# Performance work log

Measured on AMD Instinct MI355X. Metric: run time of the kernel, lower is better.

The kernel has to match this reference:

```python
import jax, jax.numpy as jnp
import numpy as np

B, S, D = 4, 4096, 64   # batch, seq_len, input_size
H, HD = 4, 16           # num_heads, head_dim


def setup_inputs() -> dict:
    key = jax.random.key(0)
    ks = jax.random.split(key, 9)
    sd = 1.0 / np.sqrt(D)          # torch Linear default uniform(-1/sqrt(fan_in), ...)
    so = 1.0 / np.sqrt(H * HD)
    u = lambda k, shape, s: jax.random.uniform(k, shape, jnp.float32, -s, s)
    return {
        "x": jax.random.normal(ks[0], (B, S, D), jnp.float32),
        "Wq": u(ks[1], (H, D, HD), sd), "bq": u(ks[2], (H, HD), sd),
        "Wk": u(ks[3], (H, D, HD), sd), "bk": u(ks[4], (H, HD), sd),
        "Wv": u(ks[5], (H, D, HD), sd), "bv": u(ks[6], (H, HD), sd),
        "Wo": u(ks[7], (H * HD, D), so), "bo": u(ks[8], (D,), so),
    }


def reference(x, Wq, bq, Wk, bk, Wv, bv, Wo, bo):
    # Batched per-head projections (fuses the original per-head Linear loop)
    q = jnp.einsum('bsd,hde->bhse', x, Wq) + bq[None, :, None, :]
    k = jnp.einsum('bsd,hde->bhse', x, Wk) + bk[None, :, None, :]
    v = jnp.einsum('bsd,hde->bhse', x, Wv) + bv[None, :, None, :]
    # scores: [B, H, S(query), S(key)]
    scores = jnp.einsum('bhse,bhte->bhst', q, k) / np.sqrt(HD).astype(np.float32)
    # FAITHFUL quirk: torch Softmax(dim=1) on [B,S,S] normalizes over the QUERY axis
    w = jax.nn.softmax(scores, axis=2)
    attended = jnp.einsum('bhst,bhte->bhse', w, v)          # [B,H,S,HD]
    concat = attended.transpose(0, 2, 1, 3).reshape(B, S, H * HD)
    out = concat @ Wo + bo                                   # [B,S,D]
    # FAITHFUL quirk: final softmax over the sequence axis (dim=1)
    return jax.nn.softmax(out, axis=1)
```

## Files before the change

### kernel.cpp

```cpp
#include <hip/hip_runtime.h>
#include <hip/hip_bf16.h>


#define BB 4
#define SS 4096
#define DD 64
#define HH 4
#define HDD 16

typedef unsigned int u32;
typedef unsigned short u16;
typedef __attribute__((ext_vector_type(8))) short bfrag;
typedef __attribute__((ext_vector_type(4))) float floatx4;
typedef __attribute__((ext_vector_type(16))) float floatx16;
typedef __attribute__((ext_vector_type(2))) u32 u32x2;
typedef __attribute__((ext_vector_type(4))) u32 u32x4;

#define LOG2E 1.4426950408889634074f
#define QSCALE (LOG2E * 0.25f)

__device__ __forceinline__ float fexp2(float x) {
#if __has_builtin(__builtin_amdgcn_exp2f)
  return __builtin_amdgcn_exp2f(x);
#else
  float r; asm("v_exp_f32 %0, %1" : "=v"(r) : "v"(x)); return r;
#endif
}
__device__ __forceinline__ float frcp(float x) {
#if __has_builtin(__builtin_amdgcn_rcpf)
  return __builtin_amdgcn_rcpf(x);
#else
  float r; asm("v_rcp_f32 %0, %1" : "=v"(r) : "v"(x)); return r;
#endif
}

__device__ __forceinline__ u16 f2bf(float f) {
  u32 u = __builtin_bit_cast(u32, f);
  return (u16)((u + 0x7FFFu + ((u >> 16) & 1u)) >> 16);
}
__device__ __forceinline__ u32 pack_bf(float lo, float hi) {
#if __has_builtin(__builtin_amdgcn_perm)
  return __builtin_amdgcn_perm(__builtin_bit_cast(u32, hi),
                               __builtin_bit_cast(u32, lo), 0x07060302u);
#else
  u32 a = __builtin_bit_cast(u32, lo);
  u32 b = __builtin_bit_cast(u32, hi);
  return (a >> 16) | (b & 0xFFFF0000u);
#endif
}

__global__ __launch_bounds__(256) void k_proj(
    const float* __restrict__ x,
    const float* __restrict__ Wq, const float* __restrict__ bq,
    const float* __restrict__ Wk, const float* __restrict__ bk,
    const float* __restrict__ Wv, const float* __restrict__ bv,
    u16* __restrict__ qb, u16* __restrict__ kb, float* __restrict__ vf)
{
  __shared__ float xs[16 * 64];
  const int tid = threadIdx.x;
  const int blk = blockIdx.x;
  const int b   = blk >> 8;
  const int s0  = (blk & 255) << 4;
  ((float4*)xs)[tid] = ((const float4*)(x + ((size_t)b * SS + s0) * DD))[tid];
  __syncthreads();

  const int col = tid & 63, h = col >> 4, e = col & 15;
  const int rg  = tid >> 6;
  float aq[4] = {0,0,0,0}, ak[4] = {0,0,0,0}, av[4] = {0,0,0,0};
  const int wofs = h * (DD * HDD) + e;
#pragma unroll 4
  for (int d = 0; d < DD; ++d) {
    float wq = Wq[wofs + d * HDD];
    float wk = Wk[wofs + d * HDD];
    float wv = Wv[wofs + d * HDD];
    const float* xr = xs + (rg * 4) * 64 + d;
#pragma unroll
    for (int r = 0; r < 4; ++r) {
      float xv = xr[r * 64];
      aq[r] += xv * wq; ak[r] += xv * wk; av[r] += xv * wv;
    }
  }
  const float bqv = bq[col], bkv = bk[col], bvv = bv[col];
  size_t base = ((size_t)(b * HH + h) * SS + (s0 + rg * 4)) * HDD + e;
#pragma unroll
  for (int r = 0; r < 4; ++r) {
    qb[base + r * HDD] = f2bf((aq[r] + bqv) * QSCALE);
    kb[base + r * HDD] = f2bf(ak[r] + bkv);
    vf[base + r * HDD] = av[r] + bvv;
  }
}

__global__ __launch_bounds__(256, 8) void k_colsum(
    const u16* __restrict__ qb, const u16* __restrict__ kb,
    float* __restrict__ csp)
{
  const int tid = threadIdx.x;
  const int lane = tid & 63, w = tid >> 6;
  const int l31 = lane & 31, hl = lane >> 5;
  const int bh = blockIdx.z, chunk = blockIdx.y;
  const int t0 = blockIdx.x * 128 + w * 32;
  const size_t base = (size_t)bh * (SS * HDD);

  const bfrag kf = *(const bfrag*)(kb + base + (size_t)(t0 + l31) * HDD + hl * 8);
  const u16* qp = qb + base + (size_t)l31 * HDD + hl * 8;
  const floatx16 z16 = {0.f};
  float c0 = 0.f, c1 = 0.f, c2 = 0.f, c3 = 0.f;
  const int s0 = chunk * 1024;
#pragma unroll 2
  for (int s = s0; s < s0 + 1024; s += 32) {
    bfrag qfr = *(const bfrag*)(qp + (size_t)s * HDD);
    floatx16 d = __builtin_amdgcn_mfma_f32_32x32x16_bf16(qfr, kf, z16, 0, 0, 0);
#pragma unroll
    for (int i = 0; i < 4; ++i) {
      c0 += fexp2(d[4 * i + 0]);
      c1 += fexp2(d[4 * i + 1]);
      c2 += fexp2(d[4 * i + 2]);
      c3 += fexp2(d[4 * i + 3]);
    }
  }
  float c = (c0 + c1) + (c2 + c3);
  c += __shfl_xor(c, 32, 64);
  if (hl == 0)
    csp[((size_t)bh * 4 + chunk) * SS + t0 + l31] = c;
}

__global__ __launch_bounds__(256, 4) void k_attn(
    const u16* __restrict__ qb, const u16* __restrict__ kb,
    const float* __restrict__ vf, const float* __restrict__ csp,
    float* __restrict__ attp)
{
  __shared__ __align__(16) u16 vls[2][16][264];
  __shared__ float rcs[2048];
  const int tid  = threadIdx.x;
  const int lane = tid & 63, w = tid >> 6;
  const int l31 = lane & 31, hl = lane >> 5;
  const int bh = blockIdx.z, b = bh >> 2, h = bh & 3;
  const int tph = blockIdx.y;
  const int s0 = blockIdx.x * 128 + w * 32;
  const size_t base = (size_t)bh * (SS * HDD);
  const int tbh = tph * 2048;

  {
    const float* cp0 = csp + (size_t)bh * 4 * SS + tbh;
#pragma unroll
    for (int i = 0; i < 8; ++i) {
      int j = i * 256 + tid;
      rcs[j] = frcp(cp0[j] + cp0[j + SS] + cp0[j + 2 * SS] + cp0[j + 3 * SS]);
    }
  }
  __syncthreads();

  const bfrag qf = *(const bfrag*)(qb + base + (size_t)(s0 + l31) * HDD + hl * 8);
  const u16* kp = kb + base + (size_t)l31 * HDD + hl * 8;
  const floatx16 z16 = {0.f};
  floatx16 acc = {0.f};

  const float4* vsrc = (const float4*)(vf + base + (size_t)tbh * HDD);

  {
#pragma unroll
    for (int kk = 0; kk < 4; ++kk) {
      int c = kk * 256 + tid;
      int tl = c >> 2, g = c & 3;
      float4 vv = vsrc[c];
      float rc = rcs[tl];
      int i5 = tl >> 5, t5 = tl & 31;
      int sub = ((t5 >> 2) & 1) * 16 + ((t5 >> 3) << 2) + (t5 & 3);
      u16* wp = &vls[0][0][0] + i5 * 32 + sub;
      wp[(4 * g + 0) * 264] = f2bf(vv.x * rc);
      wp[(4 * g + 1) * 264] = f2bf(vv.y * rc);
      wp[(4 * g + 2) * 264] = f2bf(vv.z * rc);
      wp[(4 * g + 3) * 264] = f2bf(vv.w * rc);
    }
  }
  __syncthreads();

#pragma unroll
  for (int ch = 0; ch < 8; ++ch) {
    float4 pv[4];
    if (ch < 7) {
#pragma unroll
      for (int kk = 0; kk < 4; ++kk)
        pv[kk] = vsrc[(ch + 1) * 1024 + kk * 256 + tid];
    }

    const u16* vrow = &vls[ch & 1][0][0] + (l31 & 15) * 264 + hl * 16;
    const int tb = tbh + ch * 256;
#pragma unroll 2
    for (int it = 0; it < 8; ++it) {
      bfrag kf = *(const bfrag*)(kp + (size_t)(tb + it * 32) * HDD);
      floatx16 d = __builtin_amdgcn_mfma_f32_32x32x16_bf16(kf, qf, z16, 0, 0, 0);
      u32 wr[8];
#pragma unroll
      for (int p = 0; p < 8; ++p)
        wr[p] = pack_bf(fexp2(d[2 * p]), fexp2(d[2 * p + 1]));
      const u16* va = vrow + it * 32;
      u32x4 af0 = *(const u32x4*)(va);
      u32x4 af1 = *(const u32x4*)(va + 8);
      u32x4 ef0 = {wr[0], wr[1], wr[2], wr[3]};
      u32x4 ef1 = {wr[4], wr[5], wr[6], wr[7]};
      acc = __builtin_amdgcn_mfma_f32_32x32x16_bf16(
          __builtin_bit_cast(bfrag, af0), __builtin_bit_cast(bfrag, ef0), acc, 0, 0, 0);
      acc = __builtin_amdgcn_mfma_f32_32x32x16_bf16(
          __builtin_bit_cast(bfrag, af1), __builtin_bit_cast(bfrag, ef1), acc, 0, 0, 0);
    }

    if (ch < 7) {
      u16* dstb = &vls[(ch + 1) & 1][0][0];
#pragma unroll
      for (int kk = 0; kk < 4; ++kk) {
        int c = kk * 256 + tid;
        int tl = c >> 2, g = c & 3;
        float rc = rcs[(ch + 1) * 256 + tl];
        int i5 = tl >> 5, t5 = tl & 31;
        int sub = ((t5 >> 2) & 1) * 16 + ((t5 >> 3) << 2) + (t5 & 3);
        u16* wp = dstb + i5 * 32 + sub;
        wp[(4 * g + 0) * 264] = f2bf(pv[kk].x * rc);
        wp[(4 * g + 1) * 264] = f2bf(pv[kk].y * rc);
        wp[(4 * g + 2) * 264] = f2bf(pv[kk].z * rc);
        wp[(4 * g + 3) * 264] = f2bf(pv[kk].w * rc);
      }
    }
    __syncthreads();
  }

  float* ao = attp + (((size_t)tph * BB + b) * SS + s0 + l31) * (HH * HDD)
            + h * HDD + 4 * hl;
  float4 lo4 = {acc[0], acc[1], acc[2], acc[3]};
  float4 hi4 = {acc[4], acc[5], acc[6], acc[7]};
  *(float4*)ao       = lo4;
  *(float4*)(ao + 8) = hi4;
}

__global__ __launch_bounds__(256) void k_oproj(
    const float* __restrict__ att, const float* __restrict__ Wo,
    const float* __restrict__ bo, float* __restrict__ outp,
    float* __restrict__ part)
{
  __shared__ float wols[64 * 64];
  __shared__ float red[4][64];
  const int tid = threadIdx.x;
  const int blk = blockIdx.x;
  const int b = blk >> 9, s0 = (blk & 511) << 3;
#pragma unroll
  for (int i = 0; i < 4; ++i)
    ((float4*)wols)[tid + 256 * i] = ((const float4*)Wo)[tid + 256 * i];
  __syncthreads();

  const int d = tid & 63, sg = tid >> 6;
  const float bov = bo[d];
  const size_t so = (size_t)BB * SS * 16;
  float es = 0.f;
#pragma unroll
  for (int r = 0; r < 2; ++r) {
    int s = s0 + sg * 2 + r;
    const floatx4* row = (const floatx4*)(att + ((size_t)b * SS + s) * 64);
    float acc = bov;
#pragma unroll
    for (int j = 0; j < 16; ++j) {
      floatx4 c = row[j] + row[j + so];
      acc += c[0] * wols[(4*j+0)*64 + d] + c[1] * wols[(4*j+1)*64 + d]
           + c[2] * wols[(4*j+2)*64 + d] + c[3] * wols[(4*j+3)*64 + d];
    }
    outp[((size_t)b * SS + s) * 64 + d] = acc;
    es += fexp2(acc * LOG2E);
  }
  red[sg][d] = es;
  __syncthreads();
  if (tid < 64)
    part[((size_t)b * 512 + (blk & 511)) * 64 + tid] =
        red[0][tid] + red[1][tid] + red[2][tid] + red[3][tid];
}

__global__ __launch_bounds__(256) void k_softmax(
    const float* __restrict__ outp, const float* __restrict__ part,
    float* __restrict__ out)
{
  __shared__ float red[4][64];
  __shared__ float rs[64];
  const int tid = threadIdx.x, d = tid & 63, sg = tid >> 6;
  const int st = blockIdx.x;
  const int b = blockIdx.y;
  {
    float e = 0.f;
    const float* pp = part + ((size_t)b * 512 + sg * 128) * 64 + d;
#pragma unroll 8
    for (int c = 0; c < 128; ++c) e += pp[c * 64];
    red[sg][d] = e;
  }
  __syncthreads();
  if (tid < 64)
    rs[tid] = frcp(red[0][tid] + red[1][tid] + red[2][tid] + red[3][tid]);
  __syncthreads();
  const float r = rs[d];
  const size_t rowbase = ((size_t)b * SS + st * 64 + sg * 16) * 64 + d;
#pragma unroll 4
  for (int i = 0; i < 16; ++i)
    out[rowbase + i * 64] = fexp2(outp[rowbase + i * 64] * LOG2E) * r;
}

extern "C" void kernel_launch(void* const* d_in, const int* in_sizes, int n_in,
                              void* d_out, int out_size, void* d_ws, size_t ws_size,
                              hipStream_t stream) {
  const float* x  = (const float*)d_in[0];
  const float* Wq = (const float*)d_in[1];
  const float* bq = (const float*)d_in[2];
  const float* Wk = (const float*)d_in[3];
  const float* bk = (const float*)d_in[4];
  const float* Wv = (const float*)d_in[5];
  const float* bv = (const float*)d_in[6];
  const float* Wo = (const float*)d_in[7];
  const float* bo = (const float*)d_in[8];

  char* ws = (char*)d_ws;
  constexpr size_t QB_OFF  = 0;
  constexpr size_t KB_OFF  = (size_t)2  << 20;
  constexpr size_t VF_OFF  = (size_t)4  << 20;
  constexpr size_t CSP_OFF = (size_t)10 << 20;
  constexpr size_t ATT_OFF = (size_t)11 << 20;
  constexpr size_t OUT_OFF = (size_t)27 << 20;
  constexpr size_t PT_OFF  = (size_t)31 << 20;

  u16*   qb   = (u16*)  (ws + QB_OFF);
  u16*   kb   = (u16*)  (ws + KB_OFF);
  float* vf   = (float*)(ws + VF_OFF);
  float* csp  = (float*)(ws + CSP_OFF);
  float* attp = (float*)(ws + ATT_OFF);
  float* outp = (float*)(ws + OUT_OFF);
  float* part = (float*)(ws + PT_OFF);
  float* out  = (float*)d_out;

  hipLaunchKernelGGL(k_proj,    dim3(1024),       dim3(256), 0, stream,
                     x, Wq, bq, Wk, bk, Wv, bv, qb, kb, vf);
  hipLaunchKernelGGL(k_colsum,  dim3(32, 4, 16),  dim3(256), 0, stream, qb, kb, csp);
  hipLaunchKernelGGL(k_attn,    dim3(32, 2, 16),  dim3(256), 0, stream,
                     qb, kb, vf, csp, attp);
  hipLaunchKernelGGL(k_oproj,   dim3(2048),       dim3(256), 0, stream,
                     attp, Wo, bo, outp, part);
  hipLaunchKernelGGL(k_softmax, dim3(64, 4),      dim3(256), 0, stream, outp, part, out);
}
```

Baseline: 184.2 us.

## Precompute scaled bf16 V tiles and stream them to LDS with direct loads

Adds a k_vprep kernel that scales V by the reciprocal column sums once, converts it to bf16 and writes it in a pre-swizzled tile layout. k_attn then copies those tiles straight into LDS with global_load_lds, which removes the per-block reciprocal computation and scattered scalar LDS stores. The key range is split into 4 parts instead of 2 to double the grid, and the launch bound is raised so more blocks fit per CU. The cost is an extra kernel launch, an extra pass over V in global memory, and four partial outputs that k_oproj must now sum.

```diff
diff --git a/kernel.cpp b/kernel.cpp
--- a/kernel.cpp
+++ b/kernel.cpp
@@ -47,6 +47,18 @@
   u32 b = __builtin_bit_cast(u32, hi);
   return (a >> 16) | (b & 0xFFFF0000u);
 #endif
+}
+
+__device__ __forceinline__ void gload_lds16(const u16* g, u16* l) {
+  __builtin_amdgcn_global_load_lds(
+      (const __attribute__((address_space(1))) void*)(g),
+      (__attribute__((address_space(3))) void*)(l), 16, 0, 0);
+}
+
+__device__ __forceinline__ int tmap(int c) {
+  int c5 = c & 31;
+  return (c & ~31) + (c5 & 3) + ((c5 >> 2) & 1) * 8 + ((c5 >> 3) & 1) * 16
+       + ((c5 >> 4) & 1) * 4;
 }
 
 __global__ __launch_bounds__(256) void k_proj(
@@ -124,68 +136,81 @@
     csp[((size_t)bh * 4 + chunk) * SS + t0 + l31] = c;
 }
 
-__global__ __launch_bounds__(256, 4) void k_attn(
+__global__ __launch_bounds__(256) void k_vprep(
+    const float* __restrict__ vf, const float* __restrict__ csp,
+    u16* __restrict__ vp)
+{
+  __shared__ float rcls[256];
+  const int tid = threadIdx.x;
+  const int chunk = blockIdx.x;
+  const int bh = blockIdx.y;
+  const int t0 = chunk << 8;
+  {
+    const float* cp = csp + (size_t)bh * 4 * SS + t0 + tid;
+    rcls[tid] = frcp(cp[0] + cp[SS] + cp[2 * SS] + cp[3 * SS]);
+  }
+  __syncthreads();
+  const float* vb = vf + ((size_t)bh * SS + t0) * HDD;
+  u16* outb = vp + ((size_t)bh * 16 + chunk) * 4096;
+#pragma unroll
+  for (int gi = 0; gi < 2; ++gi) {
+    const int g = gi * 256 + tid;
+    const int e = g >> 5, gg = g & 31;
+    const int cbase = (gg ^ (e & 7)) << 3;
+    u32 r[4];
+#pragma unroll
+    for (int jj = 0; jj < 4; ++jj) {
+      int ta = tmap(cbase + 2 * jj);
+      int tb = tmap(cbase + 2 * jj + 1);
+      u16 lo = f2bf(vb[ta * HDD + e] * rcls[ta]);
+      u16 hi = f2bf(vb[tb * HDD + e] * rcls[tb]);
+      r[jj] = (u32)lo | ((u32)hi << 16);
+    }
+    u32x4 vv = {r[0], r[1], r[2], r[3]};
+    *(u32x4*)(outb + g * 8) = vv;
+  }
+}
+
+__global__ __launch_bounds__(256, 8) void k_attn(
     const u16* __restrict__ qb, const u16* __restrict__ kb,
-    const float* __restrict__ vf, const float* __restrict__ csp,
-    float* __restrict__ attp)
-{
-  __shared__ __align__(16) u16 vls[2][16][264];
-  __shared__ float rcs[2048];
+    const u16* __restrict__ vp, float* __restrict__ attp)
+{
+  __shared__ __align__(16) u16 vls[2][4096];
   const int tid  = threadIdx.x;
   const int lane = tid & 63, w = tid >> 6;
   const int l31 = lane & 31, hl = lane >> 5;
   const int bh = blockIdx.z, b = bh >> 2, h = bh & 3;
-  const int tph = blockIdx.y;
+  const int tq = blockIdx.y;
   const int s0 = blockIdx.x * 128 + w * 32;
   const size_t base = (size_t)bh * (SS * HDD);
-  const int tbh = tph * 2048;
-
-  {
-    const float* cp0 = csp + (size_t)bh * 4 * SS + tbh;
-#pragma unroll
-    for (int i = 0; i < 8; ++i) {
-      int j = i * 256 + tid;
-      rcs[j] = frcp(cp0[j] + cp0[j + SS] + cp0[j + 2 * SS] + cp0[j + 3 * SS]);
-    }
-  }
-  __syncthreads();
 
   const bfrag qf = *(const bfrag*)(qb + base + (size_t)(s0 + l31) * HDD + hl * 8);
-  const u16* kp = kb + base + (size_t)l31 * HDD + hl * 8;
+  const u16* kp = kb + base + ((size_t)tq * 1024 + l31) * HDD + hl * 8;
   const floatx16 z16 = {0.f};
   floatx16 acc = {0.f};
 
-  const float4* vsrc = (const float4*)(vf + base + (size_t)tbh * HDD);
+  const u16* vsrc = vp + ((size_t)bh * 16 + tq * 4) * 4096;
 
   {
-#pragma unroll
-    for (int kk = 0; kk < 4; ++kk) {
-      int c = kk * 256 + tid;
-      int tl = c >> 2, g = c & 3;
-      float4 vv = vsrc[c];
-      float rc = rcs[tl];
-      int i5 = tl >> 5, t5 = tl & 31;
-      int sub = ((t5 >> 2) & 1) * 16 + ((t5 >> 3) << 2) + (t5 & 3);
-      u16* wp = &vls[0][0][0] + i5 * 32 + sub;
-      wp[(4 * g + 0) * 264] = f2bf(vv.x * rc);
-      wp[(4 * g + 1) * 264] = f2bf(vv.y * rc);
-      wp[(4 * g + 2) * 264] = f2bf(vv.z * rc);
-      wp[(4 * g + 3) * 264] = f2bf(vv.w * rc);
-    }
-  }
-  __syncthreads();
-
-#pragma unroll
-  for (int ch = 0; ch < 8; ++ch) {
-    float4 pv[4];
-    if (ch < 7) {
-#pragma unroll
-      for (int kk = 0; kk < 4; ++kk)
-        pv[kk] = vsrc[(ch + 1) * 1024 + kk * 256 + tid];
-    }
-
-    const u16* vrow = &vls[ch & 1][0][0] + (l31 & 15) * 264 + hl * 16;
-    const int tb = tbh + ch * 256;
+    const u16* gs = vsrc + w * 1024 + lane * 8;
+    u16* ls = &vls[0][0] + w * 1024;
+    gload_lds16(gs, ls);
+    gload_lds16(gs + 512, ls + 512);
+  }
+  __syncthreads();
+
+#pragma unroll
+  for (int ch = 0; ch < 4; ++ch) {
+    if (ch < 3) {
+      const u16* gs = vsrc + (ch + 1) * 4096 + w * 1024 + lane * 8;
+      u16* ls = &vls[(ch + 1) & 1][0] + w * 1024;
+      gload_lds16(gs, ls);
+      gload_lds16(gs + 512, ls + 512);
+    }
+
+    const u16* vrow = &vls[ch & 1][0] + (l31 & 15) * 256;
+    const int eb = l31 & 7;
+    const int tb = ch * 256;
 #pragma unroll 2
     for (int it = 0; it < 8; ++it) {
       bfrag kf = *(const bfrag*)(kp + (size_t)(tb + it * 32) * HDD);
@@ -194,9 +219,9 @@
 #pragma unroll
       for (int p = 0; p < 8; ++p)
         wr[p] = pack_bf(fexp2(d[2 * p]), fexp2(d[2 * p + 1]));
-      const u16* va = vrow + it * 32;
-      u32x4 af0 = *(const u32x4*)(va);
-      u32x4 af1 = *(const u32x4*)(va + 8);
+      const int cc0 = it * 4 + hl * 2;
+      u32x4 af0 = *(const u32x4*)(vrow + ((cc0 ^ eb) << 3));
+      u32x4 af1 = *(const u32x4*)(vrow + (((cc0 + 1) ^ eb) << 3));
       u32x4 ef0 = {wr[0], wr[1], wr[2], wr[3]};
       u32x4 ef1 = {wr[4], wr[5], wr[6], wr[7]};
       acc = __builtin_amdgcn_mfma_f32_32x32x16_bf16(
@@ -204,27 +229,10 @@
       acc = __builtin_amdgcn_mfma_f32_32x32x16_bf16(
           __builtin_bit_cast(bfrag, af1), __builtin_bit_cast(bfrag, ef1), acc, 0, 0, 0);
     }
-
-    if (ch < 7) {
-      u16* dstb = &vls[(ch + 1) & 1][0][0];
-#pragma unroll
-      for (int kk = 0; kk < 4; ++kk) {
-        int c = kk * 256 + tid;
-        int tl = c >> 2, g = c & 3;
-        float rc = rcs[(ch + 1) * 256 + tl];
-        int i5 = tl >> 5, t5 = tl & 31;
-        int sub = ((t5 >> 2) & 1) * 16 + ((t5 >> 3) << 2) + (t5 & 3);
-        u16* wp = dstb + i5 * 32 + sub;
-        wp[(4 * g + 0) * 264] = f2bf(pv[kk].x * rc);
-        wp[(4 * g + 1) * 264] = f2bf(pv[kk].y * rc);
-        wp[(4 * g + 2) * 264] = f2bf(pv[kk].z * rc);
-        wp[(4 * g + 3) * 264] = f2bf(pv[kk].w * rc);
-      }
-    }
     __syncthreads();
   }
 
-  float* ao = attp + (((size_t)tph * BB + b) * SS + s0 + l31) * (HH * HDD)
+  float* ao = attp + (((size_t)tq * BB + b) * SS + s0 + l31) * (HH * HDD)
             + h * HDD + 4 * hl;
   float4 lo4 = {acc[0], acc[1], acc[2], acc[3]};
   float4 hi4 = {acc[4], acc[5], acc[6], acc[7]};
@@ -258,7 +266,7 @@
     float acc = bov;
 #pragma unroll
     for (int j = 0; j < 16; ++j) {
-      floatx4 c = row[j] + row[j + so];
+      floatx4 c = (row[j] + row[j + so]) + (row[j + 2 * so] + row[j + 3 * so]);
       acc += c[0] * wols[(4*j+0)*64 + d] + c[1] * wols[(4*j+1)*64 + d]
            + c[2] * wols[(4*j+2)*64 + d] + c[3] * wols[(4*j+3)*64 + d];
     }
@@ -316,7 +324,8 @@
   constexpr size_t QB_OFF  = 0;
   constexpr size_t KB_OFF  = (size_t)2  << 20;
   constexpr size_t VF_OFF  = (size_t)4  << 20;
-  constexpr size_t CSP_OFF = (size_t)10 << 20;
+  constexpr size_t CSP_OFF = (size_t)8  << 20;
+  constexpr size_t VP_OFF  = (size_t)9  << 20;
   constexpr size_t ATT_OFF = (size_t)11 << 20;
   constexpr size_t OUT_OFF = (size_t)27 << 20;
   constexpr size_t PT_OFF  = (size_t)31 << 20;
@@ -325,6 +334,7 @@
   u16*   kb   = (u16*)  (ws + KB_OFF);
   float* vf   = (float*)(ws + VF_OFF);
   float* csp  = (float*)(ws + CSP_OFF);
+  u16*   vpb  = (u16*)  (ws + VP_OFF);
   float* attp = (float*)(ws + ATT_OFF);
   float* outp = (float*)(ws + OUT_OFF);
   float* part = (float*)(ws + PT_OFF);
@@ -333,8 +343,9 @@
   hipLaunchKernelGGL(k_proj,    dim3(1024),       dim3(256), 0, stream,
                      x, Wq, bq, Wk, bk, Wv, bv, qb, kb, vf);
   hipLaunchKernelGGL(k_colsum,  dim3(32, 4, 16),  dim3(256), 0, stream, qb, kb, csp);
-  hipLaunchKernelGGL(k_attn,    dim3(32, 2, 16),  dim3(256), 0, stream,
-                     qb, kb, vf, csp, attp);
+  hipLaunchKernelGGL(k_vprep,   dim3(16, 16),     dim3(256), 0, stream, vf, csp, vpb);
+  hipLaunchKernelGGL(k_attn,    dim3(32, 4, 16),  dim3(256), 0, stream,
+                     qb, kb, vpb, attp);
   hipLaunchKernelGGL(k_oproj,   dim3(2048),       dim3(256), 0, stream,
                      attp, Wo, bo, outp, part);
   hipLaunchKernelGGL(k_softmax, dim3(64, 4),      dim3(256), 0, stream, outp, part, out);
```

Result: slower. 206.3 us (+12.0%).
